# Kernel optimization log

Hardware: AMD Instinct MI355X
Metric: run time of the kernel (lower is better)

The kernel has to match this reference:

```python
import jax, jax.numpy as jnp
import numpy as np

ROUTINGS = 3


def setup_inputs() -> dict:
    key = jax.random.key(0)
    k1, k2 = jax.random.split(key)
    B, I, D_in = 64, 512, 128   # batch, input_num_capsule, input_dim_capsule
    N, O = 32, 64               # num_capsule, dim_capsule
    x = jax.random.normal(k1, (B, I, D_in), dtype=jnp.float32)
    # he_normal-ish init for W [N, I, O, D_in]
    W = jax.random.normal(k2, (N, I, O, D_in), dtype=jnp.float32) * np.float32(np.sqrt(2.0 / D_in))
    return {"x": x, "W": W}


def reference(x, W):
    # inputs_hat[b,n,i,o] = sum_d x[b,i,d] * W[n,i,o,d]
    u = jnp.einsum('bid,niod->bnio', x, W)  # [B, N, I, O]
    b = jnp.zeros(u.shape[:3], dtype=u.dtype)  # [B, N, I]
    outputs = None
    for r in range(ROUTINGS):
        c = jax.nn.softmax(b, axis=1)                    # softmax over num_capsule axis
        outputs = jnp.einsum('bni,bnio->bno', c, u)      # [B, N, O]
        if r < ROUTINGS - 1:
            b = jnp.einsum('bno,bnio->bni', outputs, u)  # agreement update
    # faithful to source: returns capsule lengths, shape [B, N]
    return jnp.sqrt(jnp.sum(jnp.square(outputs), axis=2))
```

## Files before the change

### kernel.cpp

```cpp
#include <hip/hip_runtime.h>

typedef _Float16 half_t;
typedef __attribute__((ext_vector_type(8))) _Float16 half8;
typedef __attribute__((ext_vector_type(4))) float f32x4;

#define BB 64
#define II 512
#define DD 128
#define NN 32
#define OO 64

__device__ inline void load8u(const half_t* p, float* a) {
  half8 v = *(const half8*)p;
  #pragma unroll
  for (int e = 0; e < 8; ++e) a[e] = (float)v[e];
}

__global__ __launch_bounds__(256) void k_compute_u(
    const float* __restrict__ x, const float* __restrict__ W,
    half_t* __restrict__ u)
{
  __shared__ unsigned char AsCs[16384] __attribute__((aligned(16)));
  __shared__ half_t Bs[64*128] __attribute__((aligned(16)));
  half_t* As = (half_t*)AsCs;
  float*  Cs = (float*)AsCs;
  const int tid  = threadIdx.x;
  const int i    = blockIdx.x;
  const int n0   = blockIdx.y * 8;
  const int w    = tid >> 6;
  const int lane = tid & 63;

  for (int k = 0; k < 4; ++k) {
    int flat = tid + 256*k;
    int row  = flat >> 4;
    int c8   = flat & 15;
    const float* gp = x + ((size_t)row*II + i)*DD + c8*8;
    float4 f0 = *(const float4*)(gp);
    float4 f1 = *(const float4*)(gp + 4);
    half8 v;
    v[0]=(half_t)f0.x; v[1]=(half_t)f0.y; v[2]=(half_t)f0.z; v[3]=(half_t)f0.w;
    v[4]=(half_t)f1.x; v[5]=(half_t)f1.y; v[6]=(half_t)f1.z; v[7]=(half_t)f1.w;
    int off = (row*256 + c8*16) ^ ((row & 7) << 4);
    *(half8*)((char*)As + off) = v;
  }
  __syncthreads();

  half8 av[4];
  {
    int ra = w*16 + (lane & 15);
    #pragma unroll
    for (int kk = 0; kk < 4; ++kk) {
      int aoff = (ra*256 + kk*64 + ((lane >> 4) << 4)) ^ ((ra & 7) << 4);
      av[kk] = *(half8*)((char*)As + aoff);
    }
  }

  for (int j = 0; j < 8; ++j) {
    int n = n0 + j;
    __syncthreads();

    const float* wbase = W + (((size_t)n*II + i)*OO)*DD;
    for (int k = 0; k < 4; ++k) {
      int flat = tid + 256*k;
      int row  = flat >> 4;
      int c8   = flat & 15;
      const float* gp = wbase + row*DD + c8*8;
      float4 f0 = *(const float4*)(gp);
      float4 f1 = *(const float4*)(gp + 4);
      half8 v;
      v[0]=(half_t)f0.x; v[1]=(half_t)f0.y; v[2]=(half_t)f0.z; v[3]=(half_t)f0.w;
      v[4]=(half_t)f1.x; v[5]=(half_t)f1.y; v[6]=(half_t)f1.z; v[7]=(half_t)f1.w;
      int off = (row*256 + c8*16) ^ ((row & 7) << 4);
      *(half8*)((char*)Bs + off) = v;
    }
    __syncthreads();

    f32x4 zero = {0.f, 0.f, 0.f, 0.f};
    f32x4 acc[4];
    #pragma unroll
    for (int ot = 0; ot < 4; ++ot) acc[ot] = zero;

    #pragma unroll
    for (int kk = 0; kk < 4; ++kk) {
      #pragma unroll
      for (int ot = 0; ot < 4; ++ot) {
        int rb   = ot*16 + (lane & 15);
        int boff = (rb*256 + kk*64 + ((lane >> 4) << 4)) ^ ((rb & 7) << 4);
        half8 bv = *(half8*)((char*)Bs + boff);
        acc[ot] = __builtin_amdgcn_mfma_f32_16x16x32_f16(av[kk], bv, acc[ot], 0, 0, 0);
      }
    }

    #pragma unroll
    for (int ot = 0; ot < 4; ++ot)
      #pragma unroll
      for (int r = 0; r < 4; ++r) {
        int row = w*16 + ((lane >> 4) << 2) + r;
        int col = ot*16 + (lane & 15);
        Cs[row*64 + col] = acc[ot][r];
      }
    __syncthreads();

    for (int k = 0; k < 2; ++k) {
      int flat = tid + 256*k;
      int row  = flat >> 3;
      int c8   = flat & 7;
      const float* sp = Cs + row*64 + c8*8;
      half8 v;
      #pragma unroll
      for (int e = 0; e < 8; ++e) v[e] = (half_t)sp[e];
      *(half8*)(u + (((size_t)row*NN + n)*II + i)*OO + c8*8) = v;
    }
  }
}

__global__ __launch_bounds__(256) void k_round0(
    const half_t* __restrict__ u, float* __restrict__ out0)
{
  __shared__ float sPart[32*65];
  const int tid = threadIdx.x;
  const int bn  = blockIdx.x;
  const int ip  = tid >> 3;
  const int o8  = tid & 7;
  const half_t* base = u + (size_t)bn * (II*OO);
  float a[8];
  #pragma unroll
  for (int e = 0; e < 8; ++e) a[e] = 0.f;
  for (int i = ip; i < II; i += 32) {
    float t[8];
    load8u(base + (size_t)i*OO + o8*8, t);
    #pragma unroll
    for (int e = 0; e < 8; ++e) a[e] += t[e];
  }
  #pragma unroll
  for (int e = 0; e < 8; ++e) sPart[ip*65 + o8*8 + e] = a[e];
  for (int step = 16; step >= 1; step >>= 1) {
    __syncthreads();
    if (ip < step) {
      #pragma unroll
      for (int e = 0; e < 8; ++e)
        sPart[ip*65 + o8*8 + e] += sPart[(ip+step)*65 + o8*8 + e];
    }
  }
  __syncthreads();
  if (tid < 64) out0[(size_t)bn*OO + tid] = sPart[tid] * (1.f/32.f);
}

__global__ __launch_bounds__(256, 2) void k_round_reg(
    const half_t* __restrict__ u, const float* __restrict__ out_prev,
    float* __restrict__ part)
{
  __shared__ float sOut[NN*OO];
  __shared__ float sP[NN][16][9];
  __shared__ float sLog[16][NN+1];
  __shared__ float sC[16][NN+1];
  const int tid = threadIdx.x;
  const int ic  = blockIdx.x;
  const int b   = blockIdx.y;
  const int n   = tid >> 3;
  const int q   = tid & 7;

  for (int k = 0; k < 8; ++k) {
    int flat = tid + 256*k;
    sOut[flat] = out_prev[(size_t)b*NN*OO + flat];
  }
  float a8[8];
  #pragma unroll
  for (int e = 0; e < 8; ++e) a8[e] = 0.f;
  __syncthreads();

  const half_t* ubase = u + ((size_t)b*NN + n)*II*OO;
  for (int s = 0; s < 4; ++s) {
    const int i0 = ic*64 + s*16;
    float r[16][8];
    #pragma unroll
    for (int ii = 0; ii < 16; ++ii) {
      load8u(ubase + (size_t)(i0+ii)*OO + q*8, r[ii]);
      float acc = 0.f;
      #pragma unroll
      for (int e = 0; e < 8; ++e) acc += r[ii][e] * sOut[n*OO + q*8 + e];
      sP[n][ii][q] = acc;
    }
    __syncthreads();
    #pragma unroll
    for (int h = 0; h < 2; ++h) {
      int ii = q + h*8;
      float sum = 0.f;
      #pragma unroll
      for (int q2 = 0; q2 < 8; ++q2) sum += sP[n][ii][q2];
      sLog[ii][n] = sum;
    }
    __syncthreads();
    #pragma unroll
    for (int h = 0; h < 2; ++h) {
      int ii = q + h*8;
      float m = -1e30f;
      #pragma unroll
      for (int n2 = 0; n2 < NN; ++n2) m = fmaxf(m, sLog[ii][n2]);
      float ss = 0.f;
      #pragma unroll
      for (int n2 = 0; n2 < NN; ++n2) ss += __expf(sLog[ii][n2] - m);
      sC[ii][n] = __expf(sLog[ii][n] - m) / ss;
    }
    __syncthreads();
    #pragma unroll
    for (int ii = 0; ii < 16; ++ii) {
      float cv = sC[ii][n];
      #pragma unroll
      for (int e = 0; e < 8; ++e) a8[e] += cv * r[ii][e];
    }
  }
  float* dst = part + (((size_t)ic*BB + b)*NN + n)*OO + q*8;
  #pragma unroll
  for (int e = 0; e < 8; ++e) dst[e] = a8[e];
}

__global__ __launch_bounds__(256) void k_reduce_part(
    const float* __restrict__ part, float* __restrict__ out_next)
{
  const int j = blockIdx.x*256 + threadIdx.x;
  const size_t O = (size_t)BB*NN*OO;
  float s = 0.f;
  #pragma unroll
  for (int k = 0; k < 8; ++k) s += part[(size_t)k*O + j];
  out_next[j] = s;
}

__global__ __launch_bounds__(64) void k_reduce_len(
    const float* __restrict__ part, float* __restrict__ dout)
{
  const int bn = blockIdx.x;
  const int o  = threadIdx.x;
  const size_t O = (size_t)BB*NN*OO;
  float s = 0.f;
  #pragma unroll
  for (int k = 0; k < 8; ++k) s += part[(size_t)k*O + (size_t)bn*OO + o];
  float sq = s * s;
  #pragma unroll
  for (int d = 32; d >= 1; d >>= 1) sq += __shfl_xor(sq, d, 64);
  if (o == 0) dout[bn] = sqrtf(sq);
}

extern "C" void kernel_launch(void* const* d_in, const int* in_sizes, int n_in,
                              void* d_out, int out_size, void* d_ws, size_t ws_size,
                              hipStream_t stream)
{
  const float* x = (const float*)d_in[0];
  const float* W = (const float*)d_in[1];
  float* dout = (float*)d_out;

  const size_t U = (size_t)BB*NN*II*OO;
  const size_t O = (size_t)BB*NN*OO;

  half_t* u   = (half_t*)d_ws;
  float* out0 = (float*)((char*)d_ws + U*2);
  float* out1 = out0 + O;
  float* part = out1 + O;

  k_compute_u  <<<dim3(II, 4),  dim3(256), 0, stream>>>(x, W, u);
  k_round0     <<<dim3(BB*NN),  dim3(256), 0, stream>>>(u, out0);
  k_round_reg  <<<dim3(8, BB),  dim3(256), 0, stream>>>(u, out0, part);
  k_reduce_part<<<dim3(512),    dim3(256), 0, stream>>>(part, out1);
  k_round_reg  <<<dim3(8, BB),  dim3(256), 0, stream>>>(u, out1, part);
  k_reduce_len <<<dim3(BB*NN),  dim3(64),  0, stream>>>(part, dout);
}
```

Before: 213.3 us.

## Double-buffer W tiles in u GEMM and halve routing chunk size for occupancy

The u-computation kernel now keeps two shared-memory buffers for W. It prefetches the next capsule's W slice into registers while the current MFMA tile runs, then writes it to the other buffer, so global load latency overlaps with compute. The routing kernel processes 8 input capsules per step instead of 16. This shrinks its register array and shared memory so it can run 4 blocks per CU over a 16-chunk grid. The cost is twice as many partial sums to write and reduce, and more registers held for the prefetch in the GEMM kernel.

```diff
diff --git a/kernel.cpp b/kernel.cpp
--- a/kernel.cpp
+++ b/kernel.cpp
@@ -21,7 +21,7 @@
     half_t* __restrict__ u)
 {
   __shared__ unsigned char AsCs[16384] __attribute__((aligned(16)));
-  __shared__ half_t Bs[64*128] __attribute__((aligned(16)));
+  __shared__ half_t Bs[2][64*128] __attribute__((aligned(16)));
   half_t* As = (half_t*)AsCs;
   float*  Cs = (float*)AsCs;
   const int tid  = threadIdx.x;
@@ -30,17 +30,19 @@
   const int w    = tid >> 6;
   const int lane = tid & 63;
 
+  const int srow = tid >> 4;
+  const int sc8  = tid & 15;
+
+  #pragma unroll
   for (int k = 0; k < 4; ++k) {
-    int flat = tid + 256*k;
-    int row  = flat >> 4;
-    int c8   = flat & 15;
-    const float* gp = x + ((size_t)row*II + i)*DD + c8*8;
+    int row  = srow + 16*k;
+    const float* gp = x + ((size_t)row*II + i)*DD + sc8*8;
     float4 f0 = *(const float4*)(gp);
     float4 f1 = *(const float4*)(gp + 4);
     half8 v;
     v[0]=(half_t)f0.x; v[1]=(half_t)f0.y; v[2]=(half_t)f0.z; v[3]=(half_t)f0.w;
     v[4]=(half_t)f1.x; v[5]=(half_t)f1.y; v[6]=(half_t)f1.z; v[7]=(half_t)f1.w;
-    int off = (row*256 + c8*16) ^ ((row & 7) << 4);
+    int off = (row*256 + sc8*16) ^ ((row & 7) << 4);
     *(half8*)((char*)As + off) = v;
   }
   __syncthreads();
@@ -55,38 +57,48 @@
     }
   }
 
-  for (int j = 0; j < 8; ++j) {
-    int n = n0 + j;
-    __syncthreads();
-
-    const float* wbase = W + (((size_t)n*II + i)*OO)*DD;
+  {
+    const float* wbase = W + (((size_t)n0*II + i)*OO)*DD;
+    #pragma unroll
     for (int k = 0; k < 4; ++k) {
-      int flat = tid + 256*k;
-      int row  = flat >> 4;
-      int c8   = flat & 15;
-      const float* gp = wbase + row*DD + c8*8;
+      int row = srow + 16*k;
+      const float* gp = wbase + row*DD + sc8*8;
       float4 f0 = *(const float4*)(gp);
       float4 f1 = *(const float4*)(gp + 4);
       half8 v;
       v[0]=(half_t)f0.x; v[1]=(half_t)f0.y; v[2]=(half_t)f0.z; v[3]=(half_t)f0.w;
       v[4]=(half_t)f1.x; v[5]=(half_t)f1.y; v[6]=(half_t)f1.z; v[7]=(half_t)f1.w;
-      int off = (row*256 + c8*16) ^ ((row & 7) << 4);
-      *(half8*)((char*)Bs + off) = v;
-    }
-    __syncthreads();
-
-    f32x4 zero = {0.f, 0.f, 0.f, 0.f};
+      int off = (row*256 + sc8*16) ^ ((row & 7) << 4);
+      *(half8*)((char*)Bs[0] + off) = v;
+    }
+  }
+  __syncthreads();
+
+  int cur = 0;
+  for (int j = 0; j < 8; ++j) {
+    const int n = n0 + j;
+
+    float4 pf[8];
+    if (j < 7) {
+      const float* wnext = W + (((size_t)(n+1)*II + i)*OO)*DD;
+      #pragma unroll
+      for (int k = 0; k < 4; ++k) {
+        const float* gp = wnext + (srow + 16*k)*DD + sc8*8;
+        pf[2*k]   = *(const float4*)(gp);
+        pf[2*k+1] = *(const float4*)(gp + 4);
+      }
+    }
+
     f32x4 acc[4];
     #pragma unroll
-    for (int ot = 0; ot < 4; ++ot) acc[ot] = zero;
-
+    for (int ot = 0; ot < 4; ++ot) acc[ot] = {0.f, 0.f, 0.f, 0.f};
     #pragma unroll
     for (int kk = 0; kk < 4; ++kk) {
       #pragma unroll
       for (int ot = 0; ot < 4; ++ot) {
         int rb   = ot*16 + (lane & 15);
         int boff = (rb*256 + kk*64 + ((lane >> 4) << 4)) ^ ((rb & 7) << 4);
-        half8 bv = *(half8*)((char*)Bs + boff);
+        half8 bv = *(half8*)((char*)Bs[cur] + boff);
         acc[ot] = __builtin_amdgcn_mfma_f32_16x16x32_f16(av[kk], bv, acc[ot], 0, 0, 0);
       }
     }
@@ -101,6 +113,7 @@
       }
     __syncthreads();
 
+    #pragma unroll
     for (int k = 0; k < 2; ++k) {
       int flat = tid + 256*k;
       int row  = flat >> 3;
@@ -111,6 +124,21 @@
       for (int e = 0; e < 8; ++e) v[e] = (half_t)sp[e];
       *(half8*)(u + (((size_t)row*NN + n)*II + i)*OO + c8*8) = v;
     }
+
+    if (j < 7) {
+      #pragma unroll
+      for (int k = 0; k < 4; ++k) {
+        int row = srow + 16*k;
+        float4 f0 = pf[2*k], f1 = pf[2*k+1];
+        half8 v;
+        v[0]=(half_t)f0.x; v[1]=(half_t)f0.y; v[2]=(half_t)f0.z; v[3]=(half_t)f0.w;
+        v[4]=(half_t)f1.x; v[5]=(half_t)f1.y; v[6]=(half_t)f1.z; v[7]=(half_t)f1.w;
+        int off = (row*256 + sc8*16) ^ ((row & 7) << 4);
+        *(half8*)((char*)Bs[cur^1] + off) = v;
+      }
+    }
+    __syncthreads();
+    cur ^= 1;
   }
 }
 
@@ -146,14 +174,14 @@
   if (tid < 64) out0[(size_t)bn*OO + tid] = sPart[tid] * (1.f/32.f);
 }
 
-__global__ __launch_bounds__(256, 2) void k_round_reg(
+__global__ __launch_bounds__(256, 4) void k_round_reg(
     const half_t* __restrict__ u, const float* __restrict__ out_prev,
     float* __restrict__ part)
 {
   __shared__ float sOut[NN*OO];
-  __shared__ float sP[NN][16][9];
-  __shared__ float sLog[16][NN+1];
-  __shared__ float sC[16][NN+1];
+  __shared__ float sP[NN][8][9];
+  __shared__ float sLog[8][NN+1];
+  __shared__ float sC[8][NN+1];
   const int tid = threadIdx.x;
   const int ic  = blockIdx.x;
   const int b   = blockIdx.y;
@@ -171,10 +199,10 @@
 
   const half_t* ubase = u + ((size_t)b*NN + n)*II*OO;
   for (int s = 0; s < 4; ++s) {
-    const int i0 = ic*64 + s*16;
-    float r[16][8];
-    #pragma unroll
-    for (int ii = 0; ii < 16; ++ii) {
+    const int i0 = ic*32 + s*8;
+    float r[8][8];
+    #pragma unroll
+    for (int ii = 0; ii < 8; ++ii) {
       load8u(ubase + (size_t)(i0+ii)*OO + q*8, r[ii]);
       float acc = 0.f;
       #pragma unroll
@@ -182,29 +210,25 @@
       sP[n][ii][q] = acc;
     }
     __syncthreads();
-    #pragma unroll
-    for (int h = 0; h < 2; ++h) {
-      int ii = q + h*8;
+    {
       float sum = 0.f;
       #pragma unroll
-      for (int q2 = 0; q2 < 8; ++q2) sum += sP[n][ii][q2];
-      sLog[ii][n] = sum;
-    }
-    __syncthreads();
-    #pragma unroll
-    for (int h = 0; h < 2; ++h) {
-      int ii = q + h*8;
+      for (int q2 = 0; q2 < 8; ++q2) sum += sP[n][q][q2];
+      sLog[q][n] = sum;
+    }
+    __syncthreads();
+    {
       float m = -1e30f;
       #pragma unroll
-      for (int n2 = 0; n2 < NN; ++n2) m = fmaxf(m, sLog[ii][n2]);
+      for (int n2 = 0; n2 < NN; ++n2) m = fmaxf(m, sLog[q][n2]);
       float ss = 0.f;
       #pragma unroll
-      for (int n2 = 0; n2 < NN; ++n2) ss += __expf(sLog[ii][n2] - m);
-      sC[ii][n] = __expf(sLog[ii][n] - m) / ss;
-    }
-    __syncthreads();
-    #pragma unroll
-    for (int ii = 0; ii < 16; ++ii) {
+      for (int n2 = 0; n2 < NN; ++n2) ss += __expf(sLog[q][n2] - m);
+      sC[q][n] = __expf(sLog[q][n] - m) / ss;
+    }
+    __syncthreads();
+    #pragma unroll
+    for (int ii = 0; ii < 8; ++ii) {
       float cv = sC[ii][n];
       #pragma unroll
       for (int e = 0; e < 8; ++e) a8[e] += cv * r[ii][e];
@@ -222,7 +246,7 @@
   const size_t O = (size_t)BB*NN*OO;
   float s = 0.f;
   #pragma unroll
-  for (int k = 0; k < 8; ++k) s += part[(size_t)k*O + j];
+  for (int k = 0; k < 16; ++k) s += part[(size_t)k*O + j];
   out_next[j] = s;
 }
 
@@ -234,7 +258,7 @@
   const size_t O = (size_t)BB*NN*OO;
   float s = 0.f;
   #pragma unroll
-  for (int k = 0; k < 8; ++k) s += part[(size_t)k*O + (size_t)bn*OO + o];
+  for (int k = 0; k < 16; ++k) s += part[(size_t)k*O + (size_t)bn*OO + o];
   float sq = s * s;
   #pragma unroll
   for (int d = 32; d >= 1; d >>= 1) sq += __shfl_xor(sq, d, 64);
@@ -259,8 +283,8 @@
 
   k_compute_u  <<<dim3(II, 4),  dim3(256), 0, stream>>>(x, W, u);
   k_round0     <<<dim3(BB*NN),  dim3(256), 0, stream>>>(u, out0);
-  k_round_reg  <<<dim3(8, BB),  dim3(256), 0, stream>>>(u, out0, part);
+  k_round_reg  <<<dim3(16, BB), dim3(256), 0, stream>>>(u, out0, part);
   k_reduce_part<<<dim3(512),    dim3(256), 0, stream>>>(part, out1);
-  k_round_reg  <<<dim3(8, BB),  dim3(256), 0, stream>>>(u, out1, part);
+  k_round_reg  <<<dim3(16, BB), dim3(256), 0, stream>>>(u, out1, part);
   k_reduce_len <<<dim3(BB*NN),  dim3(64),  0, stream>>>(part, dout);
 }
```

Result: no change. 213.6 us (+0.2%).
